# Optimization experiments

Measured on AMD Instinct MI355X. Metric: run time of the kernel, lower is better.

The kernel has to match this reference:

```python
import jax, jax.numpy as jnp
import numpy as np

R_MAX = 10.0
NUM_BESSEL = 8
POLY_P = 5
EMB = 64
MLP_DIM = 256
NUM_LAYERS = 3
IN_DIM = 10
OUT_DIM = 1
N_NODES = 256
N_EDGES = 1024
N_GRAPHS = 16
# gated TP output: 0e channel carries 64 scalars + 128 gates (one per gated 1o/2e irrep)
GATE_MUL = {0: 3 * EMB, 1: EMB, 2: EMB}
L0_PATHS = [(0, 0, 0), (0, 1, 1), (0, 2, 2)]  # in_irreps = 64x0e
LN_PATHS = [(0, 0, 0), (1, 1, 0), (2, 2, 0), (0, 1, 1), (1, 0, 1), (1, 2, 1), (2, 1, 1), (0, 2, 2), (2, 0, 2), (1, 1, 2), (2, 2, 2)]

def _npaths(paths):
    d = {0: 0, 1: 0, 2: 0}
    for _, _, l3 in paths:
        d[l3] += 1
    return d

L0_NP = _npaths(L0_PATHS)
LN_NP = _npaths(LN_PATHS)
L0_NUMEL = sum(EMB * GATE_MUL[l3] for _, _, l3 in L0_PATHS)   # 20480
LN_NUMEL = sum(EMB * GATE_MUL[l3] for _, _, l3 in LN_PATHS)   # 69632

# ---- real spherical harmonics, component normalization (||Y_l||^2 = 2l+1) ----
def _sh_np(v):
    x, y, z = v[:, 0], v[:, 1], v[:, 2]
    s15 = np.sqrt(15.0)
    return {0: np.ones((v.shape[0], 1)),
            1: np.sqrt(3.0) * np.stack([x, y, z], 1),
            2: np.stack([s15 * x * y, s15 * y * z, 0.5 * np.sqrt(5.0) * (3 * z * z - 1), s15 * x * z, 0.5 * s15 * (x * x - y * y)], 1)}

def _rot(axis, t):
    c, s = np.cos(t), np.sin(t)
    R = np.eye(3)
    i, j = [(1, 2), (2, 0), (0, 1)][axis]
    R[i, i] = c; R[j, j] = c; R[i, j] = -s; R[j, i] = s
    return R

_PTS = np.random.RandomState(0).randn(64, 3)
_PTS /= np.linalg.norm(_PTS, axis=1, keepdims=True)

def _D(l, R):
    # rep matrix D with Y(Rv) = D @ Y(v), fit by least squares over sample points
    A = _sh_np(_PTS)[l]
    B = _sh_np(_PTS @ R.T)[l]
    return np.linalg.lstsq(A, B, rcond=None)[0].T

def _gen(l, axis, eps=1e-4):
    return (_D(l, _rot(axis, eps)) - _D(l, _rot(axis, -eps))) / (2 * eps)

def _cg(l1, l2, l3):
    # Clebsch-Gordan tensor as null space of the infinitesimal equivariance constraint
    d1, d2, d3 = 2 * l1 + 1, 2 * l2 + 1, 2 * l3 + 1
    rows = []
    for a in range(3):
        J1, J2, J3 = _gen(l1, a), _gen(l2, a), _gen(l3, a)
        rows.append(np.kron(J1.T, np.eye(d2 * d3)) + np.kron(np.eye(d1), np.kron(J2.T, np.eye(d3))) - np.kron(np.eye(d1 * d2), J3))
    _, _, Vh = np.linalg.svd(np.vstack(rows))
    c = Vh[-1].reshape(d1, d2, d3)
    c = c / np.linalg.norm(c)
    c = c * np.sign(c.flat[int(np.argmax(np.abs(c)))])
    return c

CG = {p: jnp.asarray(_cg(*p), jnp.float32) for p in set(LN_PATHS)}

def _sh_jax(u):
    x, y, z = u[..., 0], u[..., 1], u[..., 2]
    s15 = 15.0 ** 0.5
    return {0: jnp.ones_like(x)[:, None],
            1: (3.0 ** 0.5) * jnp.stack([x, y, z], -1),
            2: jnp.stack([s15 * x * y, s15 * y * z, 0.5 * (5.0 ** 0.5) * (3 * z * z - 1), s15 * x * z, 0.5 * s15 * (x * x - y * y)], -1)}

def _radial(r):
    # Bessel radial basis * polynomial cutoff envelope (MACE-style RadialEmbeddingBlock)
    n = jnp.arange(1, NUM_BESSEL + 1, dtype=r.dtype)
    bessel = (2.0 / R_MAX) ** 0.5 * jnp.sin(n * jnp.pi * r[:, None] / R_MAX) / r[:, None]
    x = r / R_MAX
    p = POLY_P
    env = 1.0 - 0.5 * (p + 1) * (p + 2) * x ** p + p * (p + 2) * x ** (p + 1) - 0.5 * p * (p + 1) * x ** (p + 2)
    env = env * (x < 1.0)
    return bessel * env[:, None]

def _conv(h, sh, ef, recv, send, paths, n_per, w1, b1, w2, b2):
    # TensorProductConvLayer: MLP(edge_feats) -> TP weights, CG tensor product, scatter-sum, gate
    E = ef.shape[0]
    w = jax.nn.relu(ef @ w1 + b1) @ w2 + b2  # (E, weight_numel)
    msgs = {0: 0.0, 1: 0.0, 2: 0.0}
    off = 0
    for (l1, l2, l3) in paths:
        mv = GATE_MUL[l3]
        wp = w[:, off:off + EMB * mv].reshape(E, EMB, mv)
        off += EMB * mv
        tmp = jnp.einsum('eui,ej,ijk->euk', h[l1][send], sh[l2], CG[(l1, l2, l3)])
        alpha = float(1.0 / np.sqrt(EMB * n_per[l3]))  # fan-in path normalization
        msgs[l3] = msgs[l3] + alpha * jnp.einsum('euk,euv->evk', tmp, wp)
    agg = {l: jax.ops.segment_sum(msgs[l], recv, num_segments=N_NODES) for l in msgs}
    s = agg[0][..., 0]  # (N, 192): 64 scalars + 128 gates
    return {0: jax.nn.silu(s[:, :EMB])[:, :, None],
            1: agg[1] * jax.nn.sigmoid(s[:, EMB:2 * EMB])[:, :, None],
            2: agg[2] * jax.nn.sigmoid(s[:, 2 * EMB:])[:, :, None]}

def _forward(atoms, pos, edge_index, batch, emb, l0_fc1_w, l0_fc1_b, l0_fc2_w, l0_fc2_b, fcs1_w, fcs1_b, fcs2_w, fcs2_b, pred_w1, pred_b1, pred_w2, pred_b2):
    recv, send = edge_index[0], edge_index[1]
    vec = pos[recv] - pos[send]
    r = jnp.maximum(jnp.linalg.norm(vec, axis=-1), 1e-6)
    sh = _sh_jax(vec / r[:, None])
    ef = _radial(r)
    h = {0: emb[atoms][:, :, None]}  # (N, 64, 1) scalar features
    h_new = _conv(h, sh, ef, recv, send, L0_PATHS, L0_NP, l0_fc1_w, l0_fc1_b, l0_fc2_w, l0_fc2_b)
    h_new[0] = h_new[0] + h[0]  # residual; F.pad means only scalar block overlaps
    h = h_new
    for i in range(NUM_LAYERS - 1):
        h_new = _conv(h, sh, ef, recv, send, LN_PATHS, LN_NP, fcs1_w[i], fcs1_b[i], fcs2_w[i], fcs2_b[i])
        h = {l: h_new[l] + h[l] for l in h_new}
    pooled = jax.ops.segment_sum(h[0][..., 0], batch, num_segments=N_GRAPHS)  # out[:, :emb_dim]
    return jax.nn.relu(pooled @ pred_w1 + pred_b1) @ pred_w2 + pred_b2

def setup_inputs():
    key = jax.random.key(0)
    ks = jax.random.split(key, 12)
    def lin(k, fi, fo):
        return jax.random.normal(k, (fi, fo), jnp.float32) * float(1.0 / np.sqrt(fi))
    return dict(
        atoms=jax.random.randint(ks[0], (N_NODES,), 0, IN_DIM),
        pos=jax.random.normal(ks[1], (N_NODES, 3), jnp.float32) * 2.0,
        edge_index=jax.random.randint(ks[2], (2, N_EDGES), 0, N_NODES),
        batch=jnp.sort(jax.random.randint(ks[3], (N_NODES,), 0, N_GRAPHS)),
        emb=jax.random.normal(ks[4], (IN_DIM, EMB), jnp.float32),
        l0_fc1_w=lin(ks[5], NUM_BESSEL, MLP_DIM), l0_fc1_b=jnp.zeros((MLP_DIM,), jnp.float32),
        l0_fc2_w=lin(ks[6], MLP_DIM, L0_NUMEL), l0_fc2_b=jnp.zeros((L0_NUMEL,), jnp.float32),
        fcs1_w=jax.random.normal(ks[7], (NUM_LAYERS - 1, NUM_BESSEL, MLP_DIM), jnp.float32) * float(1.0 / np.sqrt(NUM_BESSEL)),
        fcs1_b=jnp.zeros((NUM_LAYERS - 1, MLP_DIM), jnp.float32),
        fcs2_w=jax.random.normal(ks[8], (NUM_LAYERS - 1, MLP_DIM, LN_NUMEL), jnp.float32) * float(1.0 / np.sqrt(MLP_DIM)),
        fcs2_b=jnp.zeros((NUM_LAYERS - 1, LN_NUMEL), jnp.float32),
        pred_w1=lin(ks[9], EMB, EMB), pred_b1=jnp.zeros((EMB,), jnp.float32),
        pred_w2=lin(ks[10], EMB, OUT_DIM), pred_b2=jnp.zeros((OUT_DIM,), jnp.float32),
    )

def reference(atoms, pos, edge_index, batch, emb, l0_fc1_w, l0_fc1_b, l0_fc2_w, l0_fc2_b, fcs1_w, fcs1_b, fcs2_w, fcs2_b, pred_w1, pred_b1, pred_w2, pred_b2):
    return _forward(atoms, pos, edge_index, batch, emb, l0_fc1_w, l0_fc1_b, l0_fc2_w, l0_fc2_b, fcs1_w, fcs1_b, fcs2_w, fcs2_b, pred_w1, pred_b1, pred_w2, pred_b2)
```

## Files before the change

### kernel.cpp

```cpp
#include <hip/hip_runtime.h>
#include <hip/hip_bf16.h>
#include <math.h>

#define NE 1024
#define NN 256
#define NG 16
#define EMB 64
#define KD 256
#define BK 64
#define NUMEL_L0 20480
#define NUMEL_LN 69632
#define MSGW 704
#define MAXE 256

typedef __attribute__((ext_vector_type(8))) __bf16 bf16x8;
typedef __attribute__((ext_vector_type(4))) float f32x4;
typedef __attribute__((ext_vector_type(4))) unsigned int u32x4;

__device__ __align__(16) float g_sh[NE * 8];
__device__ __align__(16) float g_ef[NE * 8];
__device__ __align__(16) unsigned short g_hidb[NE * KD];
__device__ __align__(16) unsigned short g_w2t[(size_t)NUMEL_LN * KD];
__device__ __align__(16) unsigned short g_wb[(size_t)NE * NUMEL_LN];
__device__ __align__(16) float g_msgs[NE * MSGW];
__device__ __align__(16) float g_h0[NN * EMB];
__device__ __align__(16) float g_h1[NN * EMB * 3];
__device__ __align__(16) float g_h2[NN * EMB * 5];
__device__ int g_elist[NN * MAXE];
__device__ int g_ecnt[NN];
__device__ float g_cg[363];

__device__ __forceinline__ unsigned short f2b(float x) {
    __hip_bfloat16 h = __float2bfloat16(x);
    return *(unsigned short*)&h;
}
__device__ __forceinline__ float b2f(unsigned short u) {
    __hip_bfloat16 h;
    *(unsigned short*)&h = u;
    return __bfloat162float(h);
}

__device__ __forceinline__ void gld16(const void* g, void* l) {
    __builtin_amdgcn_global_load_lds(
        (const __attribute__((address_space(1))) unsigned int*)g,
        (__attribute__((address_space(3))) unsigned int*)l, 16, 0, 0);
}

struct Path { int l1, l2, d1, d2, d3, mv, off, cgoff, tmpoff; };

__constant__ Path PLN[11] = {
    {0, 0, 1, 1, 1, 192, 0,     0,   0},
    {1, 1, 3, 3, 1, 192, 12288, 1,   64},
    {2, 2, 5, 5, 1, 192, 24576, 10,  128},
    {0, 1, 1, 3, 3, 64,  36864, 35,  192},
    {1, 0, 3, 1, 3, 64,  40960, 44,  384},
    {1, 2, 3, 5, 3, 64,  45056, 53,  576},
    {2, 1, 5, 3, 3, 64,  49152, 98,  768},
    {0, 2, 1, 5, 5, 64,  53248, 143, 960},
    {2, 0, 5, 1, 5, 64,  57344, 168, 1280},
    {1, 1, 3, 3, 5, 64,  61440, 193, 1600},
    {2, 2, 5, 5, 5, 64,  65536, 238, 1920},
};
__constant__ Path PL0[3] = {
    {0, 0, 1, 1, 1, 192, 0,     0,   0},
    {0, 1, 1, 3, 3, 64,  12288, 35,  64},
    {0, 2, 1, 5, 5, 64,  16384, 143, 256},
};

__device__ void init_cg_body() {
    for (int i = 0; i < 363; i++) g_cg[i] = 0.f;
    const float K3 = 0.57735026918962576f;
    const float K5 = 0.44721359549995794f;
    const float A  = 0.31622776601683794f;
    const float B  = 0.18257418583505536f;
    const float C2 = 0.36514837167011072f;
    const float P  = 0.23904572186687872f;
    const float Q  = 0.20701966780270626f;
    const float S  = 0.11952286093343936f;
    g_cg[0] = 1.f;
    for (int i = 0; i < 3; i++) g_cg[1 + i * 3 + i] = K3;
    for (int i = 0; i < 5; i++) g_cg[10 + i * 5 + i] = K5;
    for (int i = 0; i < 3; i++) g_cg[35 + i * 3 + i] = K3;
    for (int i = 0; i < 3; i++) g_cg[44 + i * 3 + i] = K3;
    g_cg[53 + 1]  = A;  g_cg[53 + 15] = A;  g_cg[53 + 20] = A;
    g_cg[53 + 34] = A;  g_cg[53 + 11] = A;  g_cg[53 + 39] = A;
    g_cg[53 + 6]  = -B; g_cg[53 + 22] = -B; g_cg[53 + 38] = C2;
    g_cg[53 + 12] = A;  g_cg[53 + 28] = -A;
    g_cg[98 + 1]  = A;  g_cg[98 + 3]  = A;  g_cg[98 + 14] = A;
    g_cg[98 + 16] = A;  g_cg[98 + 29] = A;  g_cg[98 + 33] = A;
    g_cg[98 + 18] = -B; g_cg[98 + 22] = -B; g_cg[98 + 26] = C2;
    g_cg[98 + 36] = A;  g_cg[98 + 40] = -A;
    for (int i = 0; i < 5; i++) g_cg[143 + i * 5 + i] = K5;
    for (int i = 0; i < 5; i++) g_cg[168 + i * 5 + i] = K5;
    g_cg[193 + 5]  = A;  g_cg[193 + 15] = A;  g_cg[193 + 26] = A;
    g_cg[193 + 36] = A;  g_cg[193 + 13] = A;  g_cg[193 + 33] = A;
    g_cg[193 + 2]  = -B; g_cg[193 + 22] = -B; g_cg[193 + 42] = C2;
    g_cg[193 + 4]  = A;  g_cg[193 + 24] = -A;
    g_cg[238 + 2]   = P;  g_cg[238 + 10]  = P;  g_cg[238 + 50]  = P;
    g_cg[238 + 8]   = -Q; g_cg[238 + 16]  = -Q; g_cg[238 + 28]  = -Q;
    g_cg[238 + 40]  = -Q; g_cg[238 + 76]  = -Q; g_cg[238 + 80]  = -Q;
    g_cg[238 + 32]  = -S; g_cg[238 + 36]  = -S; g_cg[238 + 56]  = -S;
    g_cg[238 + 34]  = Q;  g_cg[238 + 46]  = Q;  g_cg[238 + 106] = Q;
    g_cg[238 + 62]  = -P;
    g_cg[238 + 74]  = P;  g_cg[238 + 114] = P;  g_cg[238 + 122] = P;
    g_cg[238 + 68]  = -S; g_cg[238 + 88]  = -S; g_cg[238 + 92]  = -S;
    g_cg[238 + 94]  = -Q; g_cg[238 + 98]  = -Q; g_cg[238 + 118] = -Q;
}

__global__ __launch_bounds__(256) void k_setup(const int* ei, const float* pos,
                                               const int* atoms, const float* emb) {
    int bid = blockIdx.x, tid = threadIdx.x;
    if (bid == 0) {
        if (tid == 0) init_cg_body();
        return;
    }
    if (bid <= 4) {
        int e = (bid - 1) * 256 + tid;
        int recv = ei[e], send = ei[NE + e];
        float vx = pos[recv * 3 + 0] - pos[send * 3 + 0];
        float vy = pos[recv * 3 + 1] - pos[send * 3 + 1];
        float vz = pos[recv * 3 + 2] - pos[send * 3 + 2];
        float rn = sqrtf(vx * vx + vy * vy + vz * vz);
        float r = fmaxf(rn, 1e-6f);
        float x = vx / r, y = vy / r, z = vz / r;
        const float S3 = 1.7320508075688772f;
        const float S15 = 3.8729833462074170f;
        const float S5H = 1.1180339887498949f;
        const float S15H = 1.9364916731037085f;
        g_sh[e * 8 + 0] = S3 * x;
        g_sh[e * 8 + 1] = S3 * y;
        g_sh[e * 8 + 2] = S3 * z;
        g_sh[e * 8 + 3] = S15 * x * y;
        g_sh[e * 8 + 4] = S15 * y * z;
        g_sh[e * 8 + 5] = S5H * (3.f * z * z - 1.f);
        g_sh[e * 8 + 6] = S15 * x * z;
        g_sh[e * 8 + 7] = S15H * (x * x - y * y);
        float xr = r * 0.1f;
        float env = 0.f;
        if (xr < 1.f) {
            float x5 = xr * xr * xr * xr * xr;
            env = 1.f - 21.f * x5 + 35.f * x5 * xr - 15.f * x5 * xr * xr;
        }
        const float SB = 0.44721359549995794f;
        const float PI = 3.14159265358979323846f;
        for (int nb = 1; nb <= 8; nb++) {
            g_ef[e * 8 + nb - 1] = SB * sinf((float)nb * PI * r * 0.1f) / r * env;
        }
        return;
    }
    if (bid <= 68) {
        int idx = (bid - 5) * 256 + tid;
        int n = idx / EMB, u = idx % EMB;
        g_h0[idx] = emb[atoms[n] * EMB + u];
        for (int k = 0; k < 3; k++) g_h1[idx * 3 + k] = 0.f;
        for (int k = 0; k < 5; k++) g_h2[idx * 5 + k] = 0.f;
        return;
    }
    {
        int n = bid - 69;
        int lane = tid & 63, w = tid >> 6;
        __shared__ int wsum[4];
        int mask = 0;
#pragma unroll
        for (int i = 0; i < 4; i++) {
            if (ei[tid * 4 + i] == n) mask |= 1 << i;
        }
        int nm = __popc(mask);
        int incl = nm;
#pragma unroll
        for (int off = 1; off < 64; off <<= 1) {
            int v = __shfl_up(incl, off);
            if (lane >= off) incl += v;
        }
        if (lane == 63) wsum[w] = incl;
        __syncthreads();
        int wbase = 0;
        for (int i = 0; i < w; i++) wbase += wsum[i];
        int base = wbase + incl - nm;
#pragma unroll
        for (int i = 0; i < 4; i++) {
            if (mask & (1 << i)) g_elist[n * MAXE + base++] = tid * 4 + i;
        }
        if (tid == 255) g_ecnt[n] = wbase + incl;
    }
}

__global__ __launch_bounds__(256) void k_w2t_hid(const float* w2, int numel,
                                                 const float* w1, const float* b1) {
    __shared__ float t[32][33];
    int bid = blockIdx.x;
    int nw2 = (numel >> 5) << 3;
    if (bid < nw2) {
        int n0 = (bid >> 3) * 32, k0 = (bid & 7) * 32;
        int tx = threadIdx.x & 31, ty = threadIdx.x >> 5;
#pragma unroll
        for (int i = 0; i < 4; i++) {
            int kl = ty * 4 + i;
            t[kl][tx] = w2[(size_t)(k0 + kl) * numel + n0 + tx];
        }
        __syncthreads();
#pragma unroll
        for (int i = 0; i < 4; i++) {
            int nl = ty * 4 + i;
            g_w2t[(size_t)(n0 + nl) * KD + k0 + tx] = f2b(t[tx][nl]);
        }
    } else {
        int e = bid - nw2, m = threadIdx.x;
        float acc = b1[m];
        for (int nb = 0; nb < 8; nb++) acc += g_ef[e * 8 + nb] * w1[nb * KD + m];
        g_hidb[e * KD + m] = f2b(fmaxf(acc, 0.f));
    }
}

__global__ __launch_bounds__(256) void k_gemm_mfma(const float* b2, int numel) {
    __shared__ unsigned short S[16384];
    int tid = threadIdx.x;
    int lane = tid & 63, wid = tid >> 6;
    int wm = wid >> 1, wn = wid & 1;
    int id = blockIdx.x;
    int xcd = id & 7;
    int q = id >> 3;
    int mb = q & 7;
    int ytile = q >> 3;
    int nt = xcd + 8 * ytile;
    int m0 = mb * 128, n0 = nt * 128;
    int fr = lane & 15;
    int ko = (lane >> 4) * 8;

    const char* gA = (const char*)g_hidb;
    const char* gB = (const char*)g_w2t;
    f32x4 acc[4][4] = {};

    for (int kst = 0; kst < 4; kst++) {
#pragma unroll
        for (int i = 0; i < 4; i++) {
            int L = wid * 4096 + i * 1024 + lane * 16;
            int row = L >> 7, p = L & 127;
            int sp = p ^ ((row & 7) << 4);
            gld16(gA + ((size_t)(m0 + row) * KD + kst * BK) * 2 + sp, (char*)S + L);
        }
#pragma unroll
        for (int i = 0; i < 4; i++) {
            int L = wid * 4096 + i * 1024 + lane * 16;
            int row = L >> 7, p = L & 127;
            int sp = p ^ ((row & 7) << 4);
            gld16(gB + ((size_t)(n0 + row) * KD + kst * BK) * 2 + sp, (char*)S + 16384 + L);
        }
        __syncthreads();
#pragma unroll
        for (int ks = 0; ks < 2; ks++) {
            int klb = ks * 64 + ko * 2;
            bf16x8 af[4], bf_[4];
#pragma unroll
            for (int f = 0; f < 4; f++) {
                int ra = wm * 64 + f * 16 + fr;
                af[f] = *(bf16x8*)((char*)S + ra * 128 + (klb ^ ((ra & 7) << 4)));
                int rb = wn * 64 + f * 16 + fr;
                bf_[f] = *(bf16x8*)((char*)S + 16384 + rb * 128 + (klb ^ ((rb & 7) << 4)));
            }
#pragma unroll
            for (int i = 0; i < 4; i++)
#pragma unroll
                for (int j = 0; j < 4; j++)
                    acc[i][j] = __builtin_amdgcn_mfma_f32_16x16x32_bf16(af[i], bf_[j], acc[i][j], 0, 0, 0);
        }
        __syncthreads();
    }

#pragma unroll
    for (int j = 0; j < 4; j++) {
        int colL = wn * 64 + j * 16 + fr;
        float bb = b2[n0 + colL];
#pragma unroll
        for (int i = 0; i < 4; i++) {
#pragma unroll
            for (int r = 0; r < 4; r++) {
                int rowL = wm * 64 + i * 16 + (lane >> 4) * 4 + r;
                *(unsigned short*)((char*)S + rowL * 256 + ((colL * 2) ^ ((rowL & 7) << 4))) =
                    f2b(acc[i][j][r] + bb);
            }
        }
    }
    __syncthreads();
    for (int c = tid; c < 2048; c += 256) {
        int row = c >> 4, p16 = (c & 15) * 16;
        u32x4 v = *(u32x4*)((char*)S + row * 256 + (p16 ^ ((row & 7) << 4)));
        *(u32x4*)((char*)(g_wb + (size_t)(m0 + row) * numel + n0) + p16) = v;
    }
}

__global__ __launch_bounds__(256) void k_contract(const int* ei, int numel, int layer0) {
    int e = blockIdx.x;
    int grp = blockIdx.y;
    int tid = threadIdx.x;
    __shared__ float tmp[1280];
    const Path* PT = layer0 ? PL0 : PLN;
    int npaths = layer0 ? 3 : 11;
    int pstart = layer0 ? grp : (grp == 0 ? 0 : (grp == 1 ? 3 : 7));
    int pend   = layer0 ? grp + 1 : (grp == 0 ? 3 : (grp == 1 ? 7 : 11));
    int tbase = PT[pstart].tmpoff;
    int tend  = (pend < npaths) ? PT[pend].tmpoff : (layer0 ? 576 : 2240);
    int ttot = tend - tbase;
    const unsigned short* wrow = g_wb + (size_t)e * numel;
    int send = ei[NE + e];

    for (int t = tid; t < ttot; t += 256) {
        int tt = t + tbase;
        int p = pend - 1;
        while (tt < PT[p].tmpoff) p--;
        Path pp = PT[p];
        int rem = tt - pp.tmpoff;
        int u = rem / pp.d3, k = rem % pp.d3;
        float acc = 0.f;
        for (int i = 0; i < pp.d1; i++) {
            float hv = (pp.l1 == 0) ? g_h0[send * EMB + u]
                     : (pp.l1 == 1) ? g_h1[(send * EMB + u) * 3 + i]
                                    : g_h2[(send * EMB + u) * 5 + i];
            for (int j = 0; j < pp.d2; j++) {
                float sv = (pp.l2 == 0) ? 1.f
                         : (pp.l2 == 1 ? g_sh[e * 8 + j] : g_sh[e * 8 + 3 + j]);
                acc += hv * sv * g_cg[pp.cgoff + (i * pp.d2 + j) * pp.d3 + k];
            }
        }
        tmp[t] = acc;
    }
    __syncthreads();

    float alpha0 = layer0 ? 0.125f : 0.07216878364870323f;
    float alpha12 = layer0 ? 0.125f : 0.0625f;
    int v3 = tid / 3, k3 = tid - v3 * 3;
    int v5a = tid / 5, k5a = tid - v5a * 5;
    int p5b = 256 + tid;
    int v5b = p5b / 5, k5b = p5b - v5b * 5;
    float a0 = 0.f, a1 = 0.f;

    for (int p = pstart; p < pend; p++) {
        Path pp = PT[p];
        int to = pp.tmpoff - tbase;
        const unsigned short* wp = wrow + pp.off;
        if (pp.d3 == 1) {
            if (tid < 192) {
#pragma unroll 16
                for (int u = 0; u < 64; u++)
                    a0 += tmp[to + u] * b2f(wp[u * 192 + tid]);
            }
        } else if (pp.d3 == 3) {
            if (tid < 192) {
#pragma unroll 16
                for (int u = 0; u < 64; u++)
                    a0 += tmp[to + u * 3 + k3] * b2f(wp[u * 64 + v3]);
            }
        } else {
#pragma unroll 16
            for (int u = 0; u < 64; u++)
                a0 += tmp[to + u * 5 + k5a] * b2f(wp[u * 64 + v5a]);
            if (tid < 64) {
#pragma unroll 16
                for (int u = 0; u < 64; u++)
                    a1 += tmp[to + u * 5 + k5b] * b2f(wp[u * 64 + v5b]);
            }
        }
    }
    if (grp == 0) {
        if (tid < 192) g_msgs[e * MSGW + tid] = alpha0 * a0;
    } else if (grp == 1) {
        if (tid < 192) g_msgs[e * MSGW + 192 + tid] = alpha12 * a0;
    } else {
        g_msgs[e * MSGW + 384 + tid] = alpha12 * a0;
        if (tid < 64) g_msgs[e * MSGW + 640 + tid] = alpha12 * a1;
    }
}

__global__ __launch_bounds__(256) void k_agggate() {
    int n = blockIdx.x, tid = threadIdx.x;
    __shared__ float agg[MSGW];
    int cnt = g_ecnt[n];
    for (int d = tid; d < MSGW; d += 256) {
        float a = 0.f;
        for (int idx = 0; idx < cnt; idx++) {
            int e = g_elist[n * MAXE + idx];
            a += g_msgs[e * MSGW + d];
        }
        agg[d] = a;
    }
    __syncthreads();
    if (tid < EMB) {
        int u = tid;
        float s0 = agg[u], s1 = agg[64 + u], s2 = agg[128 + u];
        float sg0 = 1.f / (1.f + expf(-s0));
        float g0 = s0 * sg0;
        float sg1 = 1.f / (1.f + expf(-s1));
        float sg2 = 1.f / (1.f + expf(-s2));
        g_h0[n * EMB + u] += g0;
        for (int k = 0; k < 3; k++) g_h1[(n * EMB + u) * 3 + k] += agg[192 + u * 3 + k] * sg1;
        for (int k = 0; k < 5; k++) g_h2[(n * EMB + u) * 5 + k] += agg[384 + u * 5 + k] * sg2;
    }
}

__global__ __launch_bounds__(1024) void k_poolhead(const int* batch, const float* w1,
                                                   const float* b1, const float* w2,
                                                   const float* b2, float* out) {
    __shared__ float pl[NG * EMB];
    int g = threadIdx.x >> 6, u = threadIdx.x & 63;
    float a = 0.f;
    for (int n = 0; n < NN; n++)
        if (batch[n] == g) a += g_h0[n * EMB + u];
    pl[g * EMB + u] = a;
    __syncthreads();
    float t = b1[u];
    for (int uu = 0; uu < EMB; uu++) t += pl[g * EMB + uu] * w1[uu * EMB + u];
    t = fmaxf(t, 0.f);
    float contrib = t * w2[u];
    for (int off = 32; off > 0; off >>= 1) contrib += __shfl_down(contrib, off);
    if (u == 0) out[g] = contrib + b2[0];
}

extern "C" void kernel_launch(void* const* d_in, const int* in_sizes, int n_in,
                              void* d_out, int out_size, void* d_ws, size_t ws_size,
                              hipStream_t stream) {
    const int* atoms = (const int*)d_in[0];
    const float* pos = (const float*)d_in[1];
    const int* ei = (const int*)d_in[2];
    const int* batch = (const int*)d_in[3];
    const float* emb = (const float*)d_in[4];
    const float* l0w1 = (const float*)d_in[5];
    const float* l0b1 = (const float*)d_in[6];
    const float* l0w2 = (const float*)d_in[7];
    const float* l0b2 = (const float*)d_in[8];
    const float* f1w = (const float*)d_in[9];
    const float* f1b = (const float*)d_in[10];
    const float* f2w = (const float*)d_in[11];
    const float* f2b = (const float*)d_in[12];
    const float* pw1 = (const float*)d_in[13];
    const float* pb1 = (const float*)d_in[14];
    const float* pw2 = (const float*)d_in[15];
    const float* pb2 = (const float*)d_in[16];
    float* out = (float*)d_out;

    k_setup<<<dim3(325), dim3(256), 0, stream>>>(ei, pos, atoms, emb);

    for (int layer = 0; layer < 3; layer++) {
        const float* w1 = layer == 0 ? l0w1 : f1w + (size_t)(layer - 1) * 8 * KD;
        const float* b1 = layer == 0 ? l0b1 : f1b + (size_t)(layer - 1) * KD;
        const float* w2 = layer == 0 ? l0w2 : f2w + (size_t)(layer - 1) * KD * NUMEL_LN;
        const float* b2 = layer == 0 ? l0b2 : f2b + (size_t)(layer - 1) * NUMEL_LN;
        int numel = layer == 0 ? NUMEL_L0 : NUMEL_LN;
        int layer0 = layer == 0 ? 1 : 0;
        k_w2t_hid<<<dim3((numel / 32) * 8 + NE), dim3(256), 0, stream>>>(w2, numel, w1, b1);
        k_gemm_mfma<<<dim3((numel / 128) * (NE / 128)), dim3(256), 0, stream>>>(b2, numel);
        k_contract<<<dim3(NE, 3), dim3(256), 0, stream>>>(ei, numel, layer0);
        k_agggate<<<dim3(NN), dim3(256), 0, stream>>>();
    }

    k_poolhead<<<dim3(1), dim3(1024), 0, stream>>>(batch, pw1, pb1, pw2, pb2, out);
}
```

Measured before the change: 424.2 us.

## Batch weight-transpose and radial-MLP GEMM across all layers into single launches

The edge radial MLP weights depend only on edge lengths, not on node features, so all three layers' weight transposes, hidden activations and per-edge weight GEMMs are hoisted out of the layer loop into one transpose launch and one GEMM launch. This removes per-layer launch overhead and tail effects and fills the GPU with one large grid. In exchange it needs separate buffers per layer, roughly tripling the per-edge weight storage (several hundred MB of bf16), and the larger working set can lower L2/MALL reuse when the contraction kernels read it later.

```diff
diff --git a/kernel.cpp b/kernel.cpp
--- a/kernel.cpp
+++ b/kernel.cpp
@@ -19,9 +19,13 @@
 
 __device__ __align__(16) float g_sh[NE * 8];
 __device__ __align__(16) float g_ef[NE * 8];
-__device__ __align__(16) unsigned short g_hidb[NE * KD];
-__device__ __align__(16) unsigned short g_w2t[(size_t)NUMEL_LN * KD];
-__device__ __align__(16) unsigned short g_wb[(size_t)NE * NUMEL_LN];
+__device__ __align__(16) unsigned short g_hidb[3][NE * KD];
+__device__ __align__(16) unsigned short g_w2t0[(size_t)NUMEL_L0 * KD];
+__device__ __align__(16) unsigned short g_w2t1[(size_t)NUMEL_LN * KD];
+__device__ __align__(16) unsigned short g_w2t2[(size_t)NUMEL_LN * KD];
+__device__ __align__(16) unsigned short g_wb0[(size_t)NE * NUMEL_L0];
+__device__ __align__(16) unsigned short g_wb1[(size_t)NE * NUMEL_LN];
+__device__ __align__(16) unsigned short g_wb2[(size_t)NE * NUMEL_LN];
 __device__ __align__(16) float g_msgs[NE * MSGW];
 __device__ __align__(16) float g_h0[NN * EMB];
 __device__ __align__(16) float g_h1[NN * EMB * 3];
@@ -185,13 +189,20 @@
     }
 }
 
-__global__ __launch_bounds__(256) void k_w2t_hid(const float* w2, int numel,
-                                                 const float* w1, const float* b1) {
+__global__ __launch_bounds__(256) void k_w2t_hid_all(
+        const float* l0w2, const float* f2w,
+        const float* l0w1, const float* l0b1, const float* f1w, const float* f1b) {
     __shared__ float t[32][33];
     int bid = blockIdx.x;
-    int nw2 = (numel >> 5) << 3;
-    if (bid < nw2) {
-        int n0 = (bid >> 3) * 32, k0 = (bid & 7) * 32;
+    if (bid < 39936) {
+        int layer, lbid, numel;
+        const float* w2;
+        unsigned short* dst;
+        if (bid < 5120)       { layer = 0; lbid = bid;          numel = NUMEL_L0; w2 = l0w2; dst = g_w2t0; }
+        else if (bid < 22528) { layer = 1; lbid = bid - 5120;   numel = NUMEL_LN; w2 = f2w;  dst = g_w2t1; }
+        else                  { layer = 2; lbid = bid - 22528;  numel = NUMEL_LN;
+                                w2 = f2w + (size_t)KD * NUMEL_LN; dst = g_w2t2; }
+        int n0 = (lbid >> 3) * 32, k0 = (lbid & 7) * 32;
         int tx = threadIdx.x & 31, ty = threadIdx.x >> 5;
 #pragma unroll
         for (int i = 0; i < 4; i++) {
@@ -202,24 +213,36 @@
 #pragma unroll
         for (int i = 0; i < 4; i++) {
             int nl = ty * 4 + i;
-            g_w2t[(size_t)(n0 + nl) * KD + k0 + tx] = f2b(t[tx][nl]);
+            dst[(size_t)(n0 + nl) * KD + k0 + tx] = f2b(t[tx][nl]);
         }
     } else {
-        int e = bid - nw2, m = threadIdx.x;
+        int r = bid - 39936;
+        int layer = r >> 10, e = r & 1023;
+        const float* w1 = layer == 0 ? l0w1 : f1w + (size_t)(layer - 1) * 8 * KD;
+        const float* b1 = layer == 0 ? l0b1 : f1b + (size_t)(layer - 1) * KD;
+        int m = threadIdx.x;
         float acc = b1[m];
         for (int nb = 0; nb < 8; nb++) acc += g_ef[e * 8 + nb] * w1[nb * KD + m];
-        g_hidb[e * KD + m] = f2b(fmaxf(acc, 0.f));
-    }
-}
-
-__global__ __launch_bounds__(256) void k_gemm_mfma(const float* b2, int numel) {
+        g_hidb[layer][e * KD + m] = f2b(fmaxf(acc, 0.f));
+    }
+}
+
+__global__ __launch_bounds__(256) void k_gemm_all(const float* l0b2, const float* f2b_) {
     __shared__ unsigned short S[16384];
     int tid = threadIdx.x;
     int lane = tid & 63, wid = tid >> 6;
     int wm = wid >> 1, wn = wid & 1;
     int id = blockIdx.x;
-    int xcd = id & 7;
-    int q = id >> 3;
+    int layer, lid, numel;
+    const unsigned short* hidb;
+    const unsigned short* w2t;
+    unsigned short* wb;
+    const float* b2;
+    if (id < 4352)      { layer = 2; lid = id;        numel = NUMEL_LN; hidb = g_hidb[2]; w2t = g_w2t2; wb = g_wb2; b2 = f2b_ + NUMEL_LN; }
+    else if (id < 8704) { layer = 1; lid = id - 4352; numel = NUMEL_LN; hidb = g_hidb[1]; w2t = g_w2t1; wb = g_wb1; b2 = f2b_; }
+    else                { layer = 0; lid = id - 8704; numel = NUMEL_L0; hidb = g_hidb[0]; w2t = g_w2t0; wb = g_wb0; b2 = l0b2; }
+    int xcd = lid & 7;
+    int q = lid >> 3;
     int mb = q & 7;
     int ytile = q >> 3;
     int nt = xcd + 8 * ytile;
@@ -227,8 +250,8 @@
     int fr = lane & 15;
     int ko = (lane >> 4) * 8;
 
-    const char* gA = (const char*)g_hidb;
-    const char* gB = (const char*)g_w2t;
+    const char* gA = (const char*)hidb;
+    const char* gB = (const char*)w2t;
     f32x4 acc[4][4] = {};
 
     for (int kst = 0; kst < 4; kst++) {
@@ -285,15 +308,18 @@
     for (int c = tid; c < 2048; c += 256) {
         int row = c >> 4, p16 = (c & 15) * 16;
         u32x4 v = *(u32x4*)((char*)S + row * 256 + (p16 ^ ((row & 7) << 4)));
-        *(u32x4*)((char*)(g_wb + (size_t)(m0 + row) * numel + n0) + p16) = v;
-    }
-}
-
-__global__ __launch_bounds__(256) void k_contract(const int* ei, int numel, int layer0) {
+        *(u32x4*)((char*)(wb + (size_t)(m0 + row) * numel + n0) + p16) = v;
+    }
+}
+
+__global__ __launch_bounds__(256) void k_contract(const int* ei, int layer) {
     int e = blockIdx.x;
     int grp = blockIdx.y;
     int tid = threadIdx.x;
     __shared__ float tmp[1280];
+    int layer0 = (layer == 0) ? 1 : 0;
+    int numel = layer0 ? NUMEL_L0 : NUMEL_LN;
+    const unsigned short* wbase = layer == 0 ? g_wb0 : (layer == 1 ? g_wb1 : g_wb2);
     const Path* PT = layer0 ? PL0 : PLN;
     int npaths = layer0 ? 3 : 11;
     int pstart = layer0 ? grp : (grp == 0 ? 0 : (grp == 1 ? 3 : 7));
@@ -301,7 +327,7 @@
     int tbase = PT[pstart].tmpoff;
     int tend  = (pend < npaths) ? PT[pend].tmpoff : (layer0 ? 576 : 2240);
     int ttot = tend - tbase;
-    const unsigned short* wrow = g_wb + (size_t)e * numel;
+    const unsigned short* wrow = wbase + (size_t)e * numel;
     int send = ei[NE + e];
 
     for (int t = tid; t < ttot; t += 256) {
@@ -430,7 +456,7 @@
     const float* f1w = (const float*)d_in[9];
     const float* f1b = (const float*)d_in[10];
     const float* f2w = (const float*)d_in[11];
-    const float* f2b = (const float*)d_in[12];
+    const float* f2b_ = (const float*)d_in[12];
     const float* pw1 = (const float*)d_in[13];
     const float* pb1 = (const float*)d_in[14];
     const float* pw2 = (const float*)d_in[15];
@@ -438,17 +464,11 @@
     float* out = (float*)d_out;
 
     k_setup<<<dim3(325), dim3(256), 0, stream>>>(ei, pos, atoms, emb);
+    k_w2t_hid_all<<<dim3(43008), dim3(256), 0, stream>>>(l0w2, f2w, l0w1, l0b1, f1w, f1b);
+    k_gemm_all<<<dim3(9984), dim3(256), 0, stream>>>(l0b2, f2b_);
 
     for (int layer = 0; layer < 3; layer++) {
-        const float* w1 = layer == 0 ? l0w1 : f1w + (size_t)(layer - 1) * 8 * KD;
-        const float* b1 = layer == 0 ? l0b1 : f1b + (size_t)(layer - 1) * KD;
-        const float* w2 = layer == 0 ? l0w2 : f2w + (size_t)(layer - 1) * KD * NUMEL_LN;
-        const float* b2 = layer == 0 ? l0b2 : f2b + (size_t)(layer - 1) * NUMEL_LN;
-        int numel = layer == 0 ? NUMEL_L0 : NUMEL_LN;
-        int layer0 = layer == 0 ? 1 : 0;
-        k_w2t_hid<<<dim3((numel / 32) * 8 + NE), dim3(256), 0, stream>>>(w2, numel, w1, b1);
-        k_gemm_mfma<<<dim3((numel / 128) * (NE / 128)), dim3(256), 0, stream>>>(b2, numel);
-        k_contract<<<dim3(NE, 3), dim3(256), 0, stream>>>(ei, numel, layer0);
+        k_contract<<<dim3(NE, 3), dim3(256), 0, stream>>>(ei, layer);
         k_agggate<<<dim3(NN), dim3(256), 0, stream>>>();
     }
 
```

New measurement: 474.5 us. 1.12x slower.
